# Optimization experiments

Hardware: AMD Instinct MI355X
Metric: run time of the kernel (lower is better)

## Reference

```python
import jax, jax.numpy as jnp
import numpy as np

B, S, D, H = 4, 2048, 1024, 16
HD = D // H


def setup_inputs() -> dict:
    key = jax.random.key(0)
    ks = jax.random.split(key, 12)
    sc = 0.02
    inp = {
        "q": jax.random.normal(ks[0], (B, S, D), jnp.float32),
        "k": jax.random.normal(ks[1], (B, S, D), jnp.float32),
        "v": jax.random.normal(ks[2], (B, S, D), jnp.float32),
        "mask": jnp.tril(jnp.ones((S, S), jnp.int32))[None, None],  # causal [1,1,S,S]
        "Wq": jax.random.normal(ks[3], (D, D), jnp.float32) * sc,
        "bq": jnp.zeros((D,), jnp.float32),
        "Wk": jax.random.normal(ks[4], (D, D), jnp.float32) * sc,
        "bk": jnp.zeros((D,), jnp.float32),
        "Wv": jax.random.normal(ks[5], (D, D), jnp.float32) * sc,
        "bv": jnp.zeros((D,), jnp.float32),
        "Wo": jax.random.normal(ks[6], (D, D), jnp.float32) * sc,
        "bo": jnp.zeros((D,), jnp.float32),
    }
    return inp


def reference(q, k, v, mask, Wq, bq, Wk, bk, Wv, bv, Wo, bo):
    # Linear projections (torch Linear: x @ W.T + b)
    qh = (q @ Wq.T + bq).reshape(B, S, H, HD).transpose(0, 2, 1, 3)  # [B,H,S,hd]
    kh = (k @ Wk.T + bk).reshape(B, S, H, HD).transpose(0, 2, 1, 3)
    vh = (v @ Wv.T + bv).reshape(B, S, H, HD).transpose(0, 2, 1, 3)
    score = jnp.einsum("bhqd,bhkd->bhqk", qh, kh) / jnp.sqrt(jnp.float32(HD))
    score = jnp.where(mask == 0, jnp.float32(-10000.0), score)
    attn = jax.nn.softmax(score, axis=-1)
    out = jnp.einsum("bhqk,bhkd->bhqd", attn, vh)  # [B,H,S,hd]
    out = out.transpose(0, 2, 1, 3).reshape(B, S, D)
    return out @ Wo.T + bo
```

## Files before the change

### kernel.cpp

```cpp
#include <hip/hip_runtime.h>

#define S_LEN 2048
#define D_DIM 1024
#define NB    4
#define NH    16
#define HDIM  64
#define PLD   72

typedef float  f32x4  __attribute__((ext_vector_type(4)));
typedef __bf16 bf16x4 __attribute__((ext_vector_type(4)));
typedef __bf16 bf16x8 __attribute__((ext_vector_type(8)));

static __device__ __forceinline__ f32x4 mfma16(bf16x8 a, bf16x8 b, f32x4 c) {
  return __builtin_amdgcn_mfma_f32_16x16x32_bf16(a, b, c, 0, 0, 0);
}
static __device__ __forceinline__ bf16x4 cvt4(f32x4 v) {
  return __builtin_convertvector(v, bf16x4);
}
static __device__ __forceinline__ bf16x8 cvt8(f32x4 lo, f32x4 hi) {
  bf16x4 a = cvt4(lo), b = cvt4(hi);
  bf16x8 r;
  r[0] = a[0]; r[1] = a[1]; r[2] = a[2]; r[3] = a[3];
  r[4] = b[0]; r[5] = b[1]; r[6] = b[2]; r[7] = b[3];
  return r;
}
static __device__ __forceinline__ void cp16(const void* g, void* l) {
  __builtin_amdgcn_global_load_lds(
      (const __attribute__((address_space(1))) unsigned int*)g,
      (__attribute__((address_space(3))) unsigned int*)l, 16, 0, 0);
}

__global__ __launch_bounds__(256) void conv_w(
    const float* __restrict__ Wq, const float* __restrict__ Wk,
    const float* __restrict__ Wv, const float* __restrict__ Wo,
    __bf16* __restrict__ out)
{
  const float* src;
  if (blockIdx.y == 0) src = Wq;
  else if (blockIdx.y == 1) src = Wk;
  else if (blockIdx.y == 2) src = Wv;
  else src = Wo;
  size_t i = ((size_t)blockIdx.x * 256 + threadIdx.x) * 4;
  f32x4 v = *(const f32x4*)(src + i);
  *(bf16x4*)(out + (size_t)blockIdx.y * (D_DIM * D_DIM) + i) = cvt4(v);
}

__global__ __launch_bounds__(256, 2) void proj_gemm(
    const float* __restrict__ qin, const float* __restrict__ kin, const float* __restrict__ vin,
    const __bf16* __restrict__ Wbf,
    const float* __restrict__ bq, const float* __restrict__ bk, const float* __restrict__ bv,
    __bf16* __restrict__ qh, __bf16* __restrict__ kh, __bf16* __restrict__ vt)
{
  const float* A; const float* bias;
  if (blockIdx.z == 0)      { A = qin; bias = bq; }
  else if (blockIdx.z == 1) { A = kin; bias = bk; }
  else                      { A = vin; bias = bv; }
  const __bf16* W = Wbf + (size_t)blockIdx.z * (D_DIM * D_DIM);

  __shared__ float  As[128 * 64];
  __shared__ __bf16 Bs[128 * 64];

  const int tid  = threadIdx.x;
  const int wave = tid >> 6;
  const int lane = tid & 63;
  const int l15  = lane & 15;
  const int quad = lane >> 4;
  const int mbase = blockIdx.x * 128;
  const int nbase = blockIdx.y * 128;
  const int wm = (wave & 1) * 64;
  const int wn = (wave >> 1) * 64;

  const int arow = lane >> 4;
  const int brow = lane >> 3;

  f32x4 acc[4][4] = {};

  for (int kt = 0; kt < D_DIM; kt += 64) {
#pragma unroll
    for (int c = 0; c < 8; ++c) {
      int rr = c * 4 + arow;
      int r  = wave * 32 + rr;
      int col = ((lane & 15) ^ (rr & 15)) * 4;
      cp16(A + (size_t)(mbase + r) * D_DIM + kt + col, As + r * 64);
    }
#pragma unroll
    for (int c = 0; c < 4; ++c) {
      int r  = wave * 32 + c * 8 + brow;
      int col = ((lane & 7) ^ (brow & 7)) * 8;
      cp16(W + (size_t)(nbase + r) * D_DIM + kt + col, Bs + r * 64);
    }
    __syncthreads();

#pragma unroll
    for (int k0 = 0; k0 < 2; ++k0) {
      bf16x8 af[4], bfr[4];
#pragma unroll
      for (int i = 0; i < 4; ++i) {
        const float* ap = As + (wm + i * 16 + l15) * 64;
        int c0 = k0 * 8 + quad * 2;
        f32x4 lo = *(const f32x4*)(ap + ((c0 ^ l15) * 4));
        f32x4 hi = *(const f32x4*)(ap + (((c0 + 1) ^ l15) * 4));
        af[i] = cvt8(lo, hi);
        bfr[i] = *(const bf16x8*)(Bs + (wn + i * 16 + l15) * 64 +
                                  (((k0 * 4 + quad) ^ (l15 & 7)) * 8));
      }
#pragma unroll
      for (int mt = 0; mt < 4; ++mt)
#pragma unroll
        for (int nt = 0; nt < 4; ++nt)
          acc[mt][nt] = mfma16(af[mt], bfr[nt], acc[mt][nt]);
    }
    __syncthreads();
  }

  const float scl = (blockIdx.z == 0) ? 0.125f : 1.0f;
#pragma unroll
  for (int mt = 0; mt < 4; ++mt)
#pragma unroll
    for (int nt = 0; nt < 4; ++nt) {
      int n = nbase + wn + nt * 16 + l15;
      int h = n >> 6, hd = n & 63;
      float bb = bias[n];
      f32x4 vv = acc[mt][nt];
#pragma unroll
      for (int r = 0; r < 4; ++r) vv[r] = (vv[r] + bb) * scl;
      bf16x4 pv = cvt4(vv);
      int m0 = mbase + wm + mt * 16 + quad * 4;
      int b = m0 >> 11, s0 = m0 & 2047;
      if (blockIdx.z == 2) {
        *(bf16x4*)(vt + ((size_t)((b * NH + h) * HDIM + hd)) * S_LEN + s0) = pv;
      } else {
        __bf16* out = (blockIdx.z == 0) ? qh : kh;
#pragma unroll
        for (int r = 0; r < 4; ++r)
          out[((size_t)(b * NH + h) * S_LEN + s0 + r) * HDIM + hd] = pv[r];
      }
    }
}

__global__ __launch_bounds__(256, 3) void attn_kernel(
    const __bf16* __restrict__ qh, const __bf16* __restrict__ kh,
    const __bf16* __restrict__ vt, __bf16* __restrict__ ao)
{
  __shared__ __bf16 Kb[2][64 * 64];
  __shared__ __bf16 Vb[2][64 * 64];
  __shared__ __bf16 Ps[4][16 * PLD];

  const int bh = blockIdx.y;
  const int x  = blockIdx.x;
  const __bf16* qp = qh + (size_t)bh * S_LEN * HDIM;
  const __bf16* kp = kh + (size_t)bh * S_LEN * HDIM;
  const __bf16* vp = vt + (size_t)bh * HDIM * S_LEN;

  const int tid  = threadIdx.x;
  const int wave = tid >> 6;
  const int lane = tid & 63;
  const int l15  = lane & 15;
  const int quad = lane >> 4;
  const int w16  = wave * 16;
  const int srow = lane >> 3;
  const int scol = ((lane & 7) ^ srow) * 8;
  const int swz  = l15 & 7;
  const int b = bh >> 4, h = bh & 15;

  __bf16* wps = &Ps[wave][0];

  for (int ph = 0; ph < 2; ++ph) {
    const int qc = ph ? (31 - x) : x;
    const int qb = qc * 64;

    bf16x8 fq[2];
    {
      const __bf16* qrow = qp + (size_t)(qb + w16 + l15) * HDIM;
      fq[0] = *(const bf16x8*)(qrow + quad * 8);
      fq[1] = *(const bf16x8*)(qrow + 32 + quad * 8);
    }
    f32x4 accO[4] = {};
    float l_run[4] = {0.f, 0.f, 0.f, 0.f};

    __syncthreads();
#pragma unroll
    for (int c = 0; c < 2; ++c) {
      int rb = w16 + c * 8;
      cp16(kp + (size_t)(rb + srow) * HDIM + scol,  &Kb[0][rb * 64]);
      cp16(vp + (size_t)(rb + srow) * S_LEN + scol, &Vb[0][rb * 64]);
    }

    for (int kt = 0; kt <= qc; ++kt) {
      __syncthreads();
      if (kt < qc) {
        int nb = (kt + 1) & 1;
        int kbase = (kt + 1) * 64;
#pragma unroll
        for (int c = 0; c < 2; ++c) {
          int rb = w16 + c * 8;
          cp16(kp + (size_t)(kbase + rb + srow) * HDIM + scol,  &Kb[nb][rb * 64]);
          cp16(vp + (size_t)(rb + srow) * S_LEN + kbase + scol, &Vb[nb][rb * 64]);
        }
      }
      const __bf16* Kt = &Kb[kt & 1][0];
      const __bf16* Vv = &Vb[kt & 1][0];

      f32x4 sc[4] = {};
#pragma unroll
      for (int k0 = 0; k0 < 2; ++k0)
#pragma unroll
        for (int nt = 0; nt < 4; ++nt) {
          bf16x8 bk = *(const bf16x8*)(Kt + (nt * 16 + l15) * 64 + (((k0 * 4 + quad) ^ swz) * 8));
          sc[nt] = mfma16(fq[k0], bk, sc[nt]);
        }

      const bool diag = (kt == qc);
#pragma unroll
      for (int nt = 0; nt < 4; ++nt) {
        f32x4 p;
#pragma unroll
        for (int r = 0; r < 4; ++r) {
          float pv = __expf(sc[nt][r]);
          if (diag && (nt * 16 + l15 > w16 + quad * 4 + r)) pv = 0.f;
          l_run[r] += pv;
          p[r] = pv;
        }
        bf16x4 pb = cvt4(p);
#pragma unroll
        for (int r = 0; r < 4; ++r)
          wps[(quad * 4 + r) * PLD + nt * 16 + l15] = pb[r];
      }

#pragma unroll
      for (int k0 = 0; k0 < 2; ++k0) {
        bf16x8 ap = *(const bf16x8*)(wps + l15 * PLD + k0 * 32 + quad * 8);
#pragma unroll
        for (int nt = 0; nt < 4; ++nt) {
          bf16x8 bv = *(const bf16x8*)(Vv + (nt * 16 + l15) * 64 + (((k0 * 4 + quad) ^ swz) * 8));
          accO[nt] = mfma16(ap, bv, accO[nt]);
        }
      }
    }

#pragma unroll
    for (int r = 0; r < 4; ++r) {
      float s = l_run[r];
      s += __shfl_xor(s, 1); s += __shfl_xor(s, 2);
      s += __shfl_xor(s, 4); s += __shfl_xor(s, 8);
      l_run[r] = s;
    }
#pragma unroll
    for (int nt = 0; nt < 4; ++nt) {
      f32x4 ov;
#pragma unroll
      for (int r = 0; r < 4; ++r) ov[r] = accO[nt][r] / l_run[r];
      bf16x4 ob = cvt4(ov);
#pragma unroll
      for (int r = 0; r < 4; ++r) {
        int sr = qb + w16 + quad * 4 + r;
        ao[((size_t)b * S_LEN + sr) * D_DIM + h * HDIM + nt * 16 + l15] = ob[r];
      }
    }
  }
}

__global__ __launch_bounds__(256, 2) void out_gemm(
    const __bf16* __restrict__ Ain, const __bf16* __restrict__ Wbf,
    const float* __restrict__ bo, float* __restrict__ Cout)
{
  __shared__ __bf16 As[128 * 64];
  __shared__ __bf16 Bs[128 * 64];

  const int tid  = threadIdx.x;
  const int wave = tid >> 6;
  const int lane = tid & 63;
  const int l15  = lane & 15;
  const int quad = lane >> 4;
  const int mbase = blockIdx.x * 128;
  const int nbase = blockIdx.y * 128;
  const int wm = (wave & 1) * 64;
  const int wn = (wave >> 1) * 64;
  const int brow = lane >> 3;
  const int scol = ((lane & 7) ^ (brow & 7)) * 8;
  const int swz  = l15 & 7;

  f32x4 acc[4][4] = {};

  for (int kt = 0; kt < D_DIM; kt += 64) {
#pragma unroll
    for (int c = 0; c < 4; ++c) {
      int r = wave * 32 + c * 8 + brow;
      cp16(Ain + (size_t)(mbase + r) * D_DIM + kt + scol, As + r * 64);
      cp16(Wbf + (size_t)(nbase + r) * D_DIM + kt + scol, Bs + r * 64);
    }
    __syncthreads();

#pragma unroll
    for (int k0 = 0; k0 < 2; ++k0) {
      bf16x8 af[4], bfr[4];
#pragma unroll
      for (int i = 0; i < 4; ++i) {
        int off = ((k0 * 4 + quad) ^ swz) * 8;
        af[i]  = *(const bf16x8*)(As + (wm + i * 16 + l15) * 64 + off);
        bfr[i] = *(const bf16x8*)(Bs + (wn + i * 16 + l15) * 64 + off);
      }
#pragma unroll
      for (int mt = 0; mt < 4; ++mt)
#pragma unroll
        for (int nt = 0; nt < 4; ++nt)
          acc[mt][nt] = mfma16(af[mt], bfr[nt], acc[mt][nt]);
    }
    __syncthreads();
  }

#pragma unroll
  for (int mt = 0; mt < 4; ++mt)
#pragma unroll
    for (int nt = 0; nt < 4; ++nt) {
      int n = nbase + wn + nt * 16 + l15;
      float bb = bo[n];
      int m0 = mbase + wm + mt * 16 + quad * 4;
#pragma unroll
      for (int r = 0; r < 4; ++r)
        Cout[(size_t)(m0 + r) * D_DIM + n] = acc[mt][nt][r] + bb;
    }
}

extern "C" void kernel_launch(void* const* d_in, const int* in_sizes, int n_in,
                              void* d_out, int out_size, void* d_ws, size_t ws_size,
                              hipStream_t stream) {
  const float* q  = (const float*)d_in[0];
  const float* k  = (const float*)d_in[1];
  const float* v  = (const float*)d_in[2];
  const float* Wq = (const float*)d_in[4];
  const float* bq = (const float*)d_in[5];
  const float* Wk = (const float*)d_in[6];
  const float* bk = (const float*)d_in[7];
  const float* Wv = (const float*)d_in[8];
  const float* bv = (const float*)d_in[9];
  const float* Wo = (const float*)d_in[10];
  const float* bo = (const float*)d_in[11];

  __bf16* ws = (__bf16*)d_ws;
  const size_t WSZ = (size_t)D_DIM * D_DIM;
  const size_t NE  = (size_t)NB * NH * S_LEN * HDIM;
  __bf16* wbf = ws;
  __bf16* qh  = ws + 4 * WSZ;
  __bf16* kh  = qh + NE;
  __bf16* vt  = kh + NE;
  __bf16* ao  = vt + NE;

  conv_w<<<dim3(1024, 4), 256, 0, stream>>>(Wq, Wk, Wv, Wo, wbf);
  proj_gemm<<<dim3(64, 8, 3), 256, 0, stream>>>(q, k, v, wbf, bq, bk, bv, qh, kh, vt);
  attn_kernel<<<dim3(16, 64), 256, 0, stream>>>(qh, kh, vt, ao);
  out_gemm<<<dim3(64, 8), 256, 0, stream>>>(ao, wbf + 3 * WSZ, bo, (float*)d_out);
}
```

Before: 348.5 us.

## Pre-convert activations to bf16, fold log2e into Q scale, single-buffer attention

```diff
diff --git a/kernel.cpp b/kernel.cpp
--- a/kernel.cpp
+++ b/kernel.cpp
@@ -6,6 +6,7 @@
 #define NH    16
 #define HDIM  64
 #define PLD   72
+#define QSCL  0.18033688011112042f
 
 typedef float  f32x4  __attribute__((ext_vector_type(4)));
 typedef __bf16 bf16x4 __attribute__((ext_vector_type(4)));
@@ -45,19 +46,59 @@
   *(bf16x4*)(out + (size_t)blockIdx.y * (D_DIM * D_DIM) + i) = cvt4(v);
 }
 
-__global__ __launch_bounds__(256, 2) void proj_gemm(
-    const float* __restrict__ qin, const float* __restrict__ kin, const float* __restrict__ vin,
-    const __bf16* __restrict__ Wbf,
+__global__ __launch_bounds__(256) void conv_a(
+    const float* __restrict__ q, const float* __restrict__ k,
+    const float* __restrict__ v, __bf16* __restrict__ out)
+{
+  const float* src;
+  if (blockIdx.y == 0) src = q;
+  else if (blockIdx.y == 1) src = k;
+  else src = v;
+  size_t i = ((size_t)blockIdx.x * 256 + threadIdx.x) * 4;
+  f32x4 x = *(const f32x4*)(src + i);
+  *(bf16x4*)(out + (size_t)blockIdx.y * ((size_t)NB * S_LEN * D_DIM) + i) = cvt4(x);
+}
+
+static __device__ __forceinline__ void proj_epilogue(
+    f32x4 (&acc)[4][4], int z, int mbase, int nbase, int wm, int wn,
+    int l15, int quad, const float* bias,
+    __bf16* qh, __bf16* kh, __bf16* vt)
+{
+  const float scl = (z == 0) ? QSCL : 1.0f;
+#pragma unroll
+  for (int mt = 0; mt < 4; ++mt)
+#pragma unroll
+    for (int nt = 0; nt < 4; ++nt) {
+      int n = nbase + wn + nt * 16 + l15;
+      int h = n >> 6, hd = n & 63;
+      float bb = bias[n];
+      f32x4 vv = acc[mt][nt];
+#pragma unroll
+      for (int r = 0; r < 4; ++r) vv[r] = (vv[r] + bb) * scl;
+      bf16x4 pv = cvt4(vv);
+      int m0 = mbase + wm + mt * 16 + quad * 4;
+      int b = m0 >> 11, s0 = m0 & 2047;
+      if (z == 2) {
+        *(bf16x4*)(vt + ((size_t)((b * NH + h) * HDIM + hd)) * S_LEN + s0) = pv;
+      } else {
+        __bf16* out = (z == 0) ? qh : kh;
+#pragma unroll
+        for (int r = 0; r < 4; ++r)
+          out[((size_t)(b * NH + h) * S_LEN + s0 + r) * HDIM + hd] = pv[r];
+      }
+    }
+}
+
+__global__ __launch_bounds__(256, 4) void proj_bf16(
+    const __bf16* __restrict__ abf, const __bf16* __restrict__ Wbf,
     const float* __restrict__ bq, const float* __restrict__ bk, const float* __restrict__ bv,
     __bf16* __restrict__ qh, __bf16* __restrict__ kh, __bf16* __restrict__ vt)
 {
-  const float* A; const float* bias;
-  if (blockIdx.z == 0)      { A = qin; bias = bq; }
-  else if (blockIdx.z == 1) { A = kin; bias = bk; }
-  else                      { A = vin; bias = bv; }
+  const __bf16* A = abf + (size_t)blockIdx.z * ((size_t)NB * S_LEN * D_DIM);
   const __bf16* W = Wbf + (size_t)blockIdx.z * (D_DIM * D_DIM);
-
-  __shared__ float  As[128 * 64];
+  const float* bias = (blockIdx.z == 0) ? bq : (blockIdx.z == 1) ? bk : bv;
+
+  __shared__ __bf16 As[128 * 64];
   __shared__ __bf16 Bs[128 * 64];
 
   const int tid  = threadIdx.x;
@@ -69,7 +110,66 @@
   const int nbase = blockIdx.y * 128;
   const int wm = (wave & 1) * 64;
   const int wn = (wave >> 1) * 64;
-
+  const int brow = lane >> 3;
+  const int scol = ((lane & 7) ^ (brow & 7)) * 8;
+  const int swz  = l15 & 7;
+
+  f32x4 acc[4][4] = {};
+
+  for (int kt = 0; kt < D_DIM; kt += 64) {
+#pragma unroll
+    for (int c = 0; c < 4; ++c) {
+      int r = wave * 32 + c * 8 + brow;
+      cp16(A + (size_t)(mbase + r) * D_DIM + kt + scol, As + r * 64);
+      cp16(W + (size_t)(nbase + r) * D_DIM + kt + scol, Bs + r * 64);
+    }
+    __syncthreads();
+
+#pragma unroll
+    for (int k0 = 0; k0 < 2; ++k0) {
+      bf16x8 af[4], bfr[4];
+#pragma unroll
+      for (int i = 0; i < 4; ++i) {
+        int off = ((k0 * 4 + quad) ^ swz) * 8;
+        af[i]  = *(const bf16x8*)(As + (wm + i * 16 + l15) * 64 + off);
+        bfr[i] = *(const bf16x8*)(Bs + (wn + i * 16 + l15) * 64 + off);
+      }
+#pragma unroll
+      for (int mt = 0; mt < 4; ++mt)
+#pragma unroll
+        for (int nt = 0; nt < 4; ++nt)
+          acc[mt][nt] = mfma16(af[mt], bfr[nt], acc[mt][nt]);
+    }
+    __syncthreads();
+  }
+
+  proj_epilogue(acc, blockIdx.z, mbase, nbase, wm, wn, l15, quad, bias, qh, kh, vt);
+}
+
+__global__ __launch_bounds__(256, 2) void proj_f32(
+    const float* __restrict__ qin, const float* __restrict__ kin, const float* __restrict__ vin,
+    const __bf16* __restrict__ Wbf,
+    const float* __restrict__ bq, const float* __restrict__ bk, const float* __restrict__ bv,
+    __bf16* __restrict__ qh, __bf16* __restrict__ kh, __bf16* __restrict__ vt)
+{
+  const float* A; const float* bias;
+  if (blockIdx.z == 0)      { A = qin; bias = bq; }
+  else if (blockIdx.z == 1) { A = kin; bias = bk; }
+  else                      { A = vin; bias = bv; }
+  const __bf16* W = Wbf + (size_t)blockIdx.z * (D_DIM * D_DIM);
+
+  __shared__ float  As[128 * 64];
+  __shared__ __bf16 Bs[128 * 64];
+
+  const int tid  = threadIdx.x;
+  const int wave = tid >> 6;
+  const int lane = tid & 63;
+  const int l15  = lane & 15;
+  const int quad = lane >> 4;
+  const int mbase = blockIdx.x * 128;
+  const int nbase = blockIdx.y * 128;
+  const int wm = (wave & 1) * 64;
+  const int wn = (wave >> 1) * 64;
   const int arow = lane >> 4;
   const int brow = lane >> 3;
 
@@ -113,37 +213,15 @@
     __syncthreads();
   }
 
-  const float scl = (blockIdx.z == 0) ? 0.125f : 1.0f;
-#pragma unroll
-  for (int mt = 0; mt < 4; ++mt)
-#pragma unroll
-    for (int nt = 0; nt < 4; ++nt) {
-      int n = nbase + wn + nt * 16 + l15;
-      int h = n >> 6, hd = n & 63;
-      float bb = bias[n];
-      f32x4 vv = acc[mt][nt];
-#pragma unroll
-      for (int r = 0; r < 4; ++r) vv[r] = (vv[r] + bb) * scl;
-      bf16x4 pv = cvt4(vv);
-      int m0 = mbase + wm + mt * 16 + quad * 4;
-      int b = m0 >> 11, s0 = m0 & 2047;
-      if (blockIdx.z == 2) {
-        *(bf16x4*)(vt + ((size_t)((b * NH + h) * HDIM + hd)) * S_LEN + s0) = pv;
-      } else {
-        __bf16* out = (blockIdx.z == 0) ? qh : kh;
-#pragma unroll
-        for (int r = 0; r < 4; ++r)
-          out[((size_t)(b * NH + h) * S_LEN + s0 + r) * HDIM + hd] = pv[r];
-      }
-    }
-}
-
-__global__ __launch_bounds__(256, 3) void attn_kernel(
+  proj_epilogue(acc, blockIdx.z, mbase, nbase, wm, wn, l15, quad, bias, qh, kh, vt);
+}
+
+__global__ __launch_bounds__(256, 4) void attn_kernel(
     const __bf16* __restrict__ qh, const __bf16* __restrict__ kh,
     const __bf16* __restrict__ vt, __bf16* __restrict__ ao)
 {
-  __shared__ __bf16 Kb[2][64 * 64];
-  __shared__ __bf16 Vb[2][64 * 64];
+  __shared__ __bf16 Kb[64 * 64];
+  __shared__ __bf16 Vb[64 * 64];
   __shared__ __bf16 Ps[4][16 * PLD];
 
   const int bh = blockIdx.y;
@@ -178,35 +256,22 @@
     f32x4 accO[4] = {};
     float l_run[4] = {0.f, 0.f, 0.f, 0.f};
 
-    __syncthreads();
-#pragma unroll
-    for (int c = 0; c < 2; ++c) {
-      int rb = w16 + c * 8;
-      cp16(kp + (size_t)(rb + srow) * HDIM + scol,  &Kb[0][rb * 64]);
-      cp16(vp + (size_t)(rb + srow) * S_LEN + scol, &Vb[0][rb * 64]);
-    }
-
     for (int kt = 0; kt <= qc; ++kt) {
       __syncthreads();
-      if (kt < qc) {
-        int nb = (kt + 1) & 1;
-        int kbase = (kt + 1) * 64;
-#pragma unroll
-        for (int c = 0; c < 2; ++c) {
-          int rb = w16 + c * 8;
-          cp16(kp + (size_t)(kbase + rb + srow) * HDIM + scol,  &Kb[nb][rb * 64]);
-          cp16(vp + (size_t)(rb + srow) * S_LEN + kbase + scol, &Vb[nb][rb * 64]);
-        }
-      }
-      const __bf16* Kt = &Kb[kt & 1][0];
-      const __bf16* Vv = &Vb[kt & 1][0];
+#pragma unroll
+      for (int c = 0; c < 2; ++c) {
+        int rb = w16 + c * 8;
+        cp16(kp + (size_t)(kt * 64 + rb + srow) * HDIM + scol,  &Kb[rb * 64]);
+        cp16(vp + (size_t)(rb + srow) * S_LEN + kt * 64 + scol, &Vb[rb * 64]);
+      }
+      __syncthreads();
 
       f32x4 sc[4] = {};
 #pragma unroll
       for (int k0 = 0; k0 < 2; ++k0)
 #pragma unroll
         for (int nt = 0; nt < 4; ++nt) {
-          bf16x8 bk = *(const bf16x8*)(Kt + (nt * 16 + l15) * 64 + (((k0 * 4 + quad) ^ swz) * 8));
+          bf16x8 bk = *(const bf16x8*)(Kb + (nt * 16 + l15) * 64 + (((k0 * 4 + quad) ^ swz) * 8));
           sc[nt] = mfma16(fq[k0], bk, sc[nt]);
         }
 
@@ -216,7 +281,7 @@
         f32x4 p;
 #pragma unroll
         for (int r = 0; r < 4; ++r) {
-          float pv = __expf(sc[nt][r]);
+          float pv = exp2f(sc[nt][r]);
           if (diag && (nt * 16 + l15 > w16 + quad * 4 + r)) pv = 0.f;
           l_run[r] += pv;
           p[r] = pv;
@@ -232,7 +297,7 @@
         bf16x8 ap = *(const bf16x8*)(wps + l15 * PLD + k0 * 32 + quad * 8);
 #pragma unroll
         for (int nt = 0; nt < 4; ++nt) {
-          bf16x8 bv = *(const bf16x8*)(Vv + (nt * 16 + l15) * 64 + (((k0 * 4 + quad) ^ swz) * 8));
+          bf16x8 bv = *(const bf16x8*)(Vb + (nt * 16 + l15) * 64 + (((k0 * 4 + quad) ^ swz) * 8));
           accO[nt] = mfma16(ap, bv, accO[nt]);
         }
       }
@@ -260,7 +325,7 @@
   }
 }
 
-__global__ __launch_bounds__(256, 2) void out_gemm(
+__global__ __launch_bounds__(256, 4) void out_gemm(
     const __bf16* __restrict__ Ain, const __bf16* __restrict__ Wbf,
     const float* __restrict__ bo, float* __restrict__ Cout)
 {
@@ -339,15 +404,24 @@
 
   __bf16* ws = (__bf16*)d_ws;
   const size_t WSZ = (size_t)D_DIM * D_DIM;
-  const size_t NE  = (size_t)NB * NH * S_LEN * HDIM;
+  const size_t NE  = (size_t)NB * S_LEN * D_DIM;
   __bf16* wbf = ws;
   __bf16* qh  = ws + 4 * WSZ;
   __bf16* kh  = qh + NE;
   __bf16* vt  = kh + NE;
   __bf16* ao  = vt + NE;
+  __bf16* abf = vt + NE;
+  const size_t NEED = (size_t)(4 * WSZ + 3 * NE + 3 * NE) * sizeof(__bf16);
+
+  const bool useBf16A = (ws_size >= NEED);
 
   conv_w<<<dim3(1024, 4), 256, 0, stream>>>(Wq, Wk, Wv, Wo, wbf);
-  proj_gemm<<<dim3(64, 8, 3), 256, 0, stream>>>(q, k, v, wbf, bq, bk, bv, qh, kh, vt);
+  if (useBf16A) {
+    conv_a<<<dim3(8192, 3), 256, 0, stream>>>(q, k, v, abf);
+    proj_bf16<<<dim3(64, 8, 3), 256, 0, stream>>>(abf, wbf, bq, bk, bv, qh, kh, vt);
+  } else {
+    proj_f32<<<dim3(64, 8, 3), 256, 0, stream>>>(q, k, v, wbf, bq, bk, bv, qh, kh, vt);
+  }
   attn_kernel<<<dim3(16, 64), 256, 0, stream>>>(qh, kh, vt, ao);
   out_gemm<<<dim3(64, 8), 256, 0, stream>>>(ao, wbf + 3 * WSZ, bo, (float*)d_out);
 }
```

Measured after the change: 339.1 us. 1.03x faster.
